# Performance work log

Hardware: AMD Instinct MI355X
Metric: run time of the kernel (lower is better)

Reference implementation:

```python
import jax, jax.numpy as jnp
import numpy as np
import math

NUM_HEADS = 20
HEAD_SIZE = 20  # newssize = 400
NEG_INF = -1e9


def setup_inputs() -> dict:
    key = jax.random.key(0)
    ks = jax.random.split(key, 10)
    B, S, L, V, D, M = 512, 100, 30, 50000, 400, 128
    user_click = jax.random.randint(ks[0], (B, S, L), 0, V)
    seq_len = jax.random.randint(ks[1], (B,), 1, S + 1)  # at least 1 valid click
    sc = 1.0 / math.sqrt(D)
    return {
        "user_click": user_click,
        "seq_len": seq_len,
        "emb_table": jax.random.normal(ks[2], (V, D), jnp.float32) * 0.02,
        "wq": jax.random.normal(ks[3], (D, D), jnp.float32) * sc,
        "wk": jax.random.normal(ks[4], (D, D), jnp.float32) * sc,
        "wv": jax.random.normal(ks[5], (D, D), jnp.float32) * sc,
        "fc1_w": jax.random.normal(ks[6], (D, M), jnp.float32) * sc,
        "fc1_b": jnp.zeros((M,), jnp.float32),
        "fc2_w": jax.random.normal(ks[7], (M, 1), jnp.float32) * (1.0 / math.sqrt(M)),
        "fc2_b": jnp.zeros((1,), jnp.float32),
    }


def reference(user_click, seq_len, emb_table, wq, wk, wv, fc1_w, fc1_b, fc2_w, fc2_b):
    B, S, L = user_click.shape
    D = emb_table.shape[1]
    H, Dh = NUM_HEADS, HEAD_SIZE

    # news encoder: mean-pooled token embeddings -> [B, S, D]
    click = jnp.take(emb_table, user_click.reshape(-1, L), axis=0).mean(axis=1)
    click = click.reshape(B, S, D)

    # mask: valid positions get +1.0 (as in the torch code), invalid -1e9
    valid = jnp.arange(S)[None, :] < seq_len[:, None]  # [B, S]
    mask = jnp.where(valid, 1.0, NEG_INF).astype(click.dtype)

    # multi-head self-attention over history
    q = (click @ wq).reshape(B, S, H, Dh).transpose(0, 2, 1, 3)
    k = (click @ wk).reshape(B, S, H, Dh).transpose(0, 2, 1, 3)
    v = (click @ wv).reshape(B, S, H, Dh).transpose(0, 2, 1, 3)
    logits = jnp.einsum("bhqd,bhkd->bhqk", q, k) / math.sqrt(Dh)
    logits = logits + mask[:, None, None, :]
    attn = jax.nn.softmax(logits, axis=-1)
    ctx = jnp.einsum("bhqk,bhkd->bhqd", attn, v)
    ctx = ctx.transpose(0, 2, 1, 3).reshape(B, S, D)  # [B, S, D]

    # additive attention pooling over history positions
    e = jnp.tanh(ctx @ fc1_w + fc1_b)            # [B, S, M]
    alpha = e @ fc2_w + fc2_b + mask[:, :, None]  # [B, S, 1]
    w = jax.nn.softmax(alpha, axis=1)
    return jnp.sum(w * ctx, axis=1)               # [B, D]
```

## Files before the change

### kernel.cpp

```cpp
#include <hip/hip_runtime.h>
#include <hip/hip_bf16.h>

using u16 = unsigned short;
using u32 = unsigned int;

#define BB 512
#define SS 100
#define LL 30
#define DD 400
#define MM 128
#define HH 20
#define DHH 20
#define SLAB 1024000ull

typedef short v8s __attribute__((ext_vector_type(8)));
typedef float v4f __attribute__((ext_vector_type(4)));

__device__ __forceinline__ float lo2f(u32 u) { return __uint_as_float(u << 16); }
__device__ __forceinline__ float hi2f(u32 u) { return __uint_as_float(u & 0xffff0000u); }
__device__ __forceinline__ float bf2f(u16 h) { return __uint_as_float(((u32)h) << 16); }
__device__ __forceinline__ u16 f2bf(float f) {
  u32 u = __float_as_uint(f);
  u += 0x7fffu + ((u >> 16) & 1u);
  return (u16)(u >> 16);
}
__device__ __forceinline__ u32 packf2(float a, float b) {
  return (u32)f2bf(a) | (((u32)f2bf(b)) << 16);
}

__global__ __launch_bounds__(256) void k_cvt(const float* __restrict__ src,
                                             u16* __restrict__ dst, int n4) {
  const int i = blockIdx.x * 256 + threadIdx.x;
  if (i < n4) {
    const float4 v = ((const float4*)src)[i];
    ((uint2*)dst)[i] = make_uint2(packf2(v.x, v.y), packf2(v.z, v.w));
  }
}

__global__ __launch_bounds__(256) void k_warm(const uint4* __restrict__ emb16,
                                              int n16, float* __restrict__ alpha,
                                              int nA, float* __restrict__ sink) {
  const int gid = blockIdx.x * 256 + threadIdx.x;
  const int stride = gridDim.x * 256;
  for (int i = gid; i < nA; i += stride) alpha[i] = 0.f;
  u32 s = 0;
  for (int i = gid; i < n16; i += stride) {
    const uint4 v = emb16[i];
    s += v.x ^ v.y ^ v.z ^ v.w;
  }
  if (s == 0x12345678u) sink[0] = 1.f;
}

__global__ __launch_bounds__(256) void k_trans_all(const float* __restrict__ wq,
    const float* __restrict__ wk, const float* __restrict__ wv,
    const float* __restrict__ f1w, u16* __restrict__ wt, u16* __restrict__ wtf) {
  __shared__ float ts[32][33];
  const int z = blockIdx.z;
  const float* src = (z == 0) ? wq : (z == 1) ? wk : (z == 2) ? wv : f1w;
  u16* dst = (z < 3) ? (wt + (size_t)z * 160000) : wtf;
  const int N = (z < 3) ? 400 : 128;
  const int K = 400;
  const int t = threadIdx.x;
  const int n0 = blockIdx.x * 32, k0 = blockIdx.y * 32;
  const int c = t & 31, r8 = t >> 5;
#pragma unroll
  for (int i = 0; i < 4; ++i) {
    const int k = k0 + r8 + i * 8, n = n0 + c;
    ts[r8 + i * 8][c] = (k < K && n < N) ? src[(size_t)k * N + n] : 0.f;
  }
  __syncthreads();
#pragma unroll
  for (int i = 0; i < 4; ++i) {
    const int n = n0 + r8 + i * 8, k = k0 + c;
    if (n < N && k < K) dst[(size_t)n * K + k] = f2bf(ts[c][r8 + i * 8]);
  }
}

__global__ __launch_bounds__(256) void k_embed(const int* __restrict__ uc,
                                               const u16* __restrict__ emb,
                                               u32* __restrict__ click) {
  const int wave = threadIdx.x >> 6, lane = threadIdx.x & 63;
  const int bs = blockIdx.x * 4 + wave;
  __shared__ int rows[4][LL];
  if (lane < LL) rows[wave][lane] = uc[(size_t)bs * LL + lane];
  __syncthreads();
  float ax[4] = {0.f, 0.f, 0.f, 0.f}, ay[4] = {0.f, 0.f, 0.f, 0.f};
  for (int l = 0; l < LL; ++l) {
    const u32* row = (const u32*)(emb + (size_t)rows[wave][l] * DD);
    const u32 a = row[lane], b = row[lane + 64], c = row[lane + 128];
    ax[0] += lo2f(a); ay[0] += hi2f(a);
    ax[1] += lo2f(b); ay[1] += hi2f(b);
    ax[2] += lo2f(c); ay[2] += hi2f(c);
    if (lane < 8) { const u32 d = row[lane + 192]; ax[3] += lo2f(d); ay[3] += hi2f(d); }
  }
  const float s = 1.0f / (float)LL;
  u32* orow = click + (size_t)bs * 200;
  orow[lane]       = packf2(ax[0] * s, ay[0] * s);
  orow[lane + 64]  = packf2(ax[1] * s, ay[1] * s);
  orow[lane + 128] = packf2(ax[2] * s, ay[2] * s);
  if (lane < 8) orow[lane + 192] = packf2(ax[3] * s, ay[3] * s);
}

__global__ __launch_bounds__(256) void k_qkv_mfma(const u16* __restrict__ A,
    const u16* __restrict__ Wt, u16* __restrict__ qo, u16* __restrict__ ko_,
    u16* __restrict__ vo) {
  __shared__ u16 As[256][40];
  __shared__ u16 Bs[80][40];
  const int t = threadIdx.x;
  const int wave = t >> 6, lane = t & 63;
  const int q = lane >> 4, l16 = lane & 15;
  const int m0 = blockIdx.x * 256;
  const int mat = blockIdx.y / 5, ntile = blockIdx.y % 5;
  const int nb = ntile * 80;
  const u16* Bt = Wt + (size_t)(mat * 400 + nb) * 400;
  u16* O = (mat == 0) ? qo : ((mat == 1) ? ko_ : vo);
  const int mw = wave * 64;

  v4f acc[4][5];
#pragma unroll
  for (int i = 0; i < 4; ++i)
#pragma unroll
    for (int j = 0; j < 5; ++j) acc[i][j] = (v4f){0.f, 0.f, 0.f, 0.f};

  for (int kt = 0; kt < 13; ++kt) {
    const int k0 = kt * 32;
#pragma unroll
    for (int i = 0; i < 4; ++i) {
      const int id = i * 256 + t;
      const int r = id >> 2, ko = (id & 3) * 8;
      uint4 val = make_uint4(0u, 0u, 0u, 0u);
      if (k0 + ko < 400) val = *(const uint4*)&A[(size_t)(m0 + r) * 400 + k0 + ko];
      *(uint4*)&As[r][ko] = val;
    }
#pragma unroll
    for (int i = 0; i < 2; ++i) {
      const int id = i * 256 + t;
      if (id < 320) {
        const int n = id >> 2, ko = (id & 3) * 8;
        uint4 val = make_uint4(0u, 0u, 0u, 0u);
        if (k0 + ko < 400) val = *(const uint4*)&Bt[(size_t)n * 400 + k0 + ko];
        *(uint4*)&Bs[n][ko] = val;
      }
    }
    __syncthreads();
    v8s a[4], b[5];
#pragma unroll
    for (int ms = 0; ms < 4; ++ms) a[ms] = *(const v8s*)&As[mw + ms * 16 + l16][q * 8];
#pragma unroll
    for (int ns = 0; ns < 5; ++ns) b[ns] = *(const v8s*)&Bs[ns * 16 + l16][q * 8];
#pragma unroll
    for (int ms = 0; ms < 4; ++ms)
#pragma unroll
      for (int ns = 0; ns < 5; ++ns)
        acc[ms][ns] = __builtin_amdgcn_mfma_f32_16x16x32_bf16(a[ms], b[ns], acc[ms][ns], 0, 0, 0);
    __syncthreads();
  }
#pragma unroll
  for (int ms = 0; ms < 4; ++ms)
#pragma unroll
    for (int ns = 0; ns < 5; ++ns) {
      const v4f c = acc[ms][ns];
      const int col = nb + ns * 16 + l16;
      const int head = col / 20, dh = col % 20;
      u16* Oh = O + (size_t)head * SLAB + dh;
#pragma unroll
      for (int reg = 0; reg < 4; ++reg) {
        const int m = m0 + mw + ms * 16 + q * 4 + reg;
        Oh[(size_t)m * 20] = f2bf(c[reg]);
      }
    }
}

__global__ __launch_bounds__(256) void k_attn_mfma(const u16* __restrict__ qg,
    const u16* __restrict__ kg, const u16* __restrict__ vg,
    const int* __restrict__ seq, u16* __restrict__ ctxg) {
  __shared__ u16 Qs[112][40];
  __shared__ u16 Ks[112][40];
  __shared__ u16 Vs[112][40];
  __shared__ u16 Vt[32][136];
  __shared__ u16 Ss[112][136];
  const int b = blockIdx.x / HH, h = blockIdx.x % HH;
  const int t = threadIdx.x;
  const int wave = t >> 6, lane = t & 63;
  const int quad = lane >> 4, l16 = lane & 15;
  const int len = seq[b];
  const u16* qb = qg + (size_t)h * SLAB + (size_t)b * SS * DHH;
  const u16* kb = kg + (size_t)h * SLAB + (size_t)b * SS * DHH;
  const u16* vb = vg + (size_t)h * SLAB + (size_t)b * SS * DHH;
  for (int id = t; id < 896; id += 256) {
    const int r = id >> 3, ch = id & 7;
    uint2 vq = make_uint2(0u, 0u), vk = vq, vv = vq;
    if (r < 100 && ch < 5) {
      vq = *(const uint2*)(qb + r * DHH + ch * 4);
      vk = *(const uint2*)(kb + r * DHH + ch * 4);
      vv = *(const uint2*)(vb + r * DHH + ch * 4);
    }
    *(uint2*)&Qs[r][ch * 4] = vq;
    *(uint2*)&Ks[r][ch * 4] = vk;
    *(uint2*)&Vs[r][ch * 4] = vv;
  }
  for (int id = t; id < 816; id += 256) ((u32*)&Vt[20][0])[id] = 0u;
  for (int id = t; id < 360; id += 256) {
    const int r = id / 18, c = id % 18;
    *(u32*)&Vt[r][100 + c * 2] = 0u;
  }
  for (int id = t; id < 896; id += 256) {
    const int r = id >> 3, c = id & 7;
    *(u32*)&Ss[r][112 + c * 2] = 0u;
  }
  __syncthreads();
  for (int id = t; id < 2000; id += 256) {
    const int d = id / 100, key = id % 100;
    Vt[d][key] = Vs[key][d];
  }
  const float sc = 0.2236067977499790f;
  for (int mi = 0; mi < 2; ++mi) {
    const int mt = wave + mi * 4;
    if (mt >= 7) break;
    const v8s a = *(const v8s*)&Qs[mt * 16 + l16][quad * 8];
    v4f acc[7];
#pragma unroll
    for (int nt = 0; nt < 7; ++nt) {
      const v8s bk = *(const v8s*)&Ks[nt * 16 + l16][quad * 8];
      acc[nt] = __builtin_amdgcn_mfma_f32_16x16x32_bf16(a, bk, (v4f){0.f,0.f,0.f,0.f}, 0, 0, 0);
    }
#pragma unroll
    for (int reg = 0; reg < 4; ++reg) {
      float v[7];
      float mx = -3.0e38f;
#pragma unroll
      for (int nt = 0; nt < 7; ++nt) {
        const int col = nt * 16 + l16;
        v[nt] = acc[nt][reg] * sc + ((col < len) ? 1.0f : -1e9f);
        mx = fmaxf(mx, v[nt]);
      }
#pragma unroll
      for (int o = 1; o < 16; o <<= 1) mx = fmaxf(mx, __shfl_xor(mx, o));
      float sum = 0.f;
#pragma unroll
      for (int nt = 0; nt < 7; ++nt) { v[nt] = __expf(v[nt] - mx); sum += v[nt]; }
#pragma unroll
      for (int o = 1; o < 16; o <<= 1) sum += __shfl_xor(sum, o);
      const float inv = 1.0f / sum;
      const int row = mt * 16 + quad * 4 + reg;
#pragma unroll
      for (int nt = 0; nt < 7; ++nt) Ss[row][nt * 16 + l16] = f2bf(v[nt] * inv);
    }
  }
  __syncthreads();
  u16* cb = ctxg + (size_t)b * SS * DD + h * DHH;
  for (int mi = 0; mi < 2; ++mi) {
    const int mt = wave + mi * 4;
    if (mt >= 7) break;
    v4f o0 = (v4f){0.f,0.f,0.f,0.f}, o1 = o0;
#pragma unroll
    for (int kc = 0; kc < 4; ++kc) {
      const v8s a  = *(const v8s*)&Ss[mt * 16 + l16][kc * 32 + quad * 8];
      const v8s b0 = *(const v8s*)&Vt[l16][kc * 32 + quad * 8];
      const v8s b1 = *(const v8s*)&Vt[16 + l16][kc * 32 + quad * 8];
      o0 = __builtin_amdgcn_mfma_f32_16x16x32_bf16(a, b0, o0, 0, 0, 0);
      o1 = __builtin_amdgcn_mfma_f32_16x16x32_bf16(a, b1, o1, 0, 0, 0);
    }
#pragma unroll
    for (int reg = 0; reg < 4; ++reg) {
      const int q = mt * 16 + quad * 4 + reg;
      if (q < 100) {
        cb[(size_t)q * DD + l16] = f2bf(o0[reg]);
        if (l16 < 4) cb[(size_t)q * DD + 16 + l16] = f2bf(o1[reg]);
      }
    }
  }
}

__global__ __launch_bounds__(256) void k_fc1_alpha(const u16* __restrict__ A,
    const u16* __restrict__ Bt, const float* __restrict__ f1b,
    const float* __restrict__ f2w, float* __restrict__ alpha) {
  __shared__ u16 As[128][40];
  __shared__ u16 Bs[64][40];
  const int t = threadIdx.x;
  const int wave = t >> 6, lane = t & 63;
  const int quad = lane >> 4, l16 = lane & 15;
  const int m0 = blockIdx.x * 128;
  const int nb = blockIdx.y * 64;
  const int mw = wave * 32;
  v4f acc[2][4];
#pragma unroll
  for (int i = 0; i < 2; ++i)
#pragma unroll
    for (int j = 0; j < 4; ++j) acc[i][j] = (v4f){0.f, 0.f, 0.f, 0.f};

  for (int kt = 0; kt < 13; ++kt) {
    const int k0 = kt * 32;
#pragma unroll
    for (int i = 0; i < 2; ++i) {
      const int id = i * 256 + t;
      const int r = id >> 2, ko = (id & 3) * 8;
      uint4 val = make_uint4(0u, 0u, 0u, 0u);
      if (k0 + ko < 400) val = *(const uint4*)&A[(size_t)(m0 + r) * 400 + k0 + ko];
      *(uint4*)&As[r][ko] = val;
    }
    {
      const int r = t >> 2, ko = (t & 3) * 8;
      uint4 val = make_uint4(0u, 0u, 0u, 0u);
      if (k0 + ko < 400) val = *(const uint4*)&Bt[(size_t)(nb + r) * 400 + k0 + ko];
      *(uint4*)&Bs[r][ko] = val;
    }
    __syncthreads();
    v8s a[2], b[4];
#pragma unroll
    for (int ms = 0; ms < 2; ++ms) a[ms] = *(const v8s*)&As[mw + ms * 16 + l16][quad * 8];
#pragma unroll
    for (int ns = 0; ns < 4; ++ns) b[ns] = *(const v8s*)&Bs[ns * 16 + l16][quad * 8];
#pragma unroll
    for (int ms = 0; ms < 2; ++ms)
#pragma unroll
      for (int ns = 0; ns < 4; ++ns)
        acc[ms][ns] = __builtin_amdgcn_mfma_f32_16x16x32_bf16(a[ms], b[ns], acc[ms][ns], 0, 0, 0);
    __syncthreads();
  }
  float fwv[4], fbv[4];
#pragma unroll
  for (int ns = 0; ns < 4; ++ns) {
    fwv[ns] = f2w[nb + ns * 16 + l16];
    fbv[ns] = f1b[nb + ns * 16 + l16];
  }
#pragma unroll
  for (int ms = 0; ms < 2; ++ms)
#pragma unroll
    for (int reg = 0; reg < 4; ++reg) {
      float p = 0.f;
#pragma unroll
      for (int ns = 0; ns < 4; ++ns)
        p += tanhf(acc[ms][ns][reg] + fbv[ns]) * fwv[ns];
#pragma unroll
      for (int o = 1; o < 16; o <<= 1) p += __shfl_xor(p, o);
      if (l16 == 0)
        atomicAdd(&alpha[m0 + mw + ms * 16 + quad * 4 + reg], p);
    }
}

__global__ __launch_bounds__(256) void k_pool(const float* __restrict__ alpha,
    const float* __restrict__ f2b, const int* __restrict__ seq,
    const u16* __restrict__ ctxg, float* __restrict__ out) {
  const int b = blockIdx.x;
  const int t = threadIdx.x, w = t >> 6, lane = t & 63;
  __shared__ float wts[SS];
  const int len = seq[b];
  const float bias = f2b[0];
  if (t < SS) wts[t] = alpha[b * SS + t] + bias + ((t < len) ? 1.0f : -1e9f);
  __syncthreads();
  if (w == 0) {
    const float v0 = wts[lane];
    const float v1 = (lane + 64 < SS) ? wts[lane + 64] : -3.0e38f;
    float mx = fmaxf(v0, v1);
#pragma unroll
    for (int o = 32; o > 0; o >>= 1) mx = fmaxf(mx, __shfl_xor(mx, o));
    const float e0 = __expf(v0 - mx);
    const float e1 = (lane + 64 < SS) ? __expf(v1 - mx) : 0.f;
    float sm = e0 + e1;
#pragma unroll
    for (int o = 32; o > 0; o >>= 1) sm += __shfl_xor(sm, o);
    const float inv = 1.0f / sm;
    wts[lane] = e0 * inv;
    if (lane + 64 < SS) wts[lane + 64] = e1 * inv;
  }
  __syncthreads();
  for (int d = t; d < DD; d += 256) {
    float acc = 0.f;
    const u16* cb = ctxg + (size_t)b * SS * DD + d;
    for (int s = 0; s < SS; ++s) acc += wts[s] * bf2f(cb[(size_t)s * DD]);
    out[(size_t)b * DD + d] = acc;
  }
}

extern "C" void kernel_launch(void* const* d_in, const int* in_sizes, int n_in,
                              void* d_out, int out_size, void* d_ws, size_t ws_size,
                              hipStream_t stream) {
  const int*   uc  = (const int*)d_in[0];
  const int*   seq = (const int*)d_in[1];
  const float* emb = (const float*)d_in[2];
  const float* wq  = (const float*)d_in[3];
  const float* wk  = (const float*)d_in[4];
  const float* wv  = (const float*)d_in[5];
  const float* f1w = (const float*)d_in[6];
  const float* f1b = (const float*)d_in[7];
  const float* f2w = (const float*)d_in[8];
  const float* f2b = (const float*)d_in[9];
  float* out = (float*)d_out;

  u16* emb16   = (u16*)d_ws;
  u16* wt      = emb16 + 20000000ull;
  u16* wtf     = wt + 480000ull;
  u16* click16 = wtf + 51200ull;
  u16* q16     = click16 + 20480000ull;
  u16* k16     = q16 + 20480000ull;
  u16* v16     = k16 + 20480000ull;
  float* alpha = (float*)(v16 + 20480000ull);
  float* sink  = alpha + 51200ull;

  k_cvt<<<(5000000 + 255) / 256, 256, 0, stream>>>(emb, emb16, 5000000);
  k_warm<<<2560, 256, 0, stream>>>((const uint4*)emb16, 2500000, alpha, 51200, sink);
  k_trans_all<<<dim3(13, 13, 4), 256, 0, stream>>>(wq, wk, wv, f1w, wt, wtf);
  k_embed<<<12800, 256, 0, stream>>>(uc, emb16, (u32*)click16);
  k_qkv_mfma<<<dim3(200, 15), 256, 0, stream>>>(click16, wt, q16, k16, v16);
  k_attn_mfma<<<BB * HH, 256, 0, stream>>>(q16, k16, v16, seq, click16);
  k_fc1_alpha<<<dim3(400, 2), 256, 0, stream>>>(click16, wtf, f1b, f2w, alpha);
  k_pool<<<BB, 256, 0, stream>>>(alpha, f2b, seq, click16, out);
}
```

Before: 642.2 us.

## Split bf16 embedding table into column slices for cache-local gather

Converts the fp32 embedding table into eight column slices of 25 packed bf16 pairs each, stored slice-major, and rewrites the gather kernel so each block handles one slice for 20 history items. The aim is to keep each slice's working set small enough to stay resident in cache during the random-row gather, and to order blocks so all eight slices of a chunk run together. The cost is that each gathered row now yields only 100 contiguous bytes per slice, which is less efficient per access. The warm-up kernel is also reordered to run after the weight transpose and to walk the slices.

After: 623.2 us. 1.03x faster.

```diff
diff --git a/kernel.cpp b/kernel.cpp
--- a/kernel.cpp
+++ b/kernel.cpp
@@ -28,24 +28,29 @@
   return (u32)f2bf(a) | (((u32)f2bf(b)) << 16);
 }
 
-__global__ __launch_bounds__(256) void k_cvt(const float* __restrict__ src,
-                                             u16* __restrict__ dst, int n4) {
-  const int i = blockIdx.x * 256 + threadIdx.x;
-  if (i < n4) {
-    const float4 v = ((const float4*)src)[i];
-    ((uint2*)dst)[i] = make_uint2(packf2(v.x, v.y), packf2(v.z, v.w));
-  }
-}
-
-__global__ __launch_bounds__(256) void k_warm(const uint4* __restrict__ emb16,
-                                              int n16, float* __restrict__ alpha,
-                                              int nA, float* __restrict__ sink) {
+__global__ __launch_bounds__(256) void k_slice(const float* __restrict__ emb,
+                                               u32* __restrict__ embS) {
+  const int tid = blockIdx.x * 256 + threadIdx.x;
+  if (tid >= 10000000) return;
+  const int c = tid % 25;
+  const int row = (tid / 25) % 50000;
+  const int slice = tid / (25 * 50000);
+  const float2 v = *(const float2*)&emb[(size_t)row * DD + (slice * 25 + c) * 2];
+  embS[tid] = packf2(v.x, v.y);
+}
+
+__global__ __launch_bounds__(256) void k_warm(const uint4* __restrict__ embS4,
+                                              float* __restrict__ alpha,
+                                              float* __restrict__ sink) {
+  const int slice = blockIdx.x & 7;
+  const int blk = blockIdx.x >> 3;
   const int gid = blockIdx.x * 256 + threadIdx.x;
-  const int stride = gridDim.x * 256;
-  for (int i = gid; i < nA; i += stride) alpha[i] = 0.f;
+  const int gstride = gridDim.x * 256;
+  for (int i = gid; i < 51200; i += gstride) alpha[i] = 0.f;
   u32 s = 0;
-  for (int i = gid; i < n16; i += stride) {
-    const uint4 v = emb16[i];
+  const int base = slice * 312500;
+  for (int i = blk * 256 + threadIdx.x; i < 312500; i += 320 * 256) {
+    const uint4 v = embS4[base + i];
     s += v.x ^ v.y ^ v.z ^ v.w;
   }
   if (s == 0x12345678u) sink[0] = 1.f;
@@ -76,29 +81,32 @@
   }
 }
 
-__global__ __launch_bounds__(256) void k_embed(const int* __restrict__ uc,
-                                               const u16* __restrict__ emb,
-                                               u32* __restrict__ click) {
-  const int wave = threadIdx.x >> 6, lane = threadIdx.x & 63;
-  const int bs = blockIdx.x * 4 + wave;
-  __shared__ int rows[4][LL];
-  if (lane < LL) rows[wave][lane] = uc[(size_t)bs * LL + lane];
-  __syncthreads();
-  float ax[4] = {0.f, 0.f, 0.f, 0.f}, ay[4] = {0.f, 0.f, 0.f, 0.f};
+__global__ __launch_bounds__(256) void k_embed_s(const int* __restrict__ uc,
+                                                 const u32* __restrict__ embS,
+                                                 u32* __restrict__ click) {
+  __shared__ int sIdx[600];
+  const int slice = blockIdx.x & 7;
+  const int chunk = blockIdx.x >> 3;
+  const int bs0 = chunk * 20;
+  const int t = threadIdx.x;
+  for (int i = t; i < 600; i += 256) sIdx[i] = uc[(size_t)bs0 * LL + i];
+  __syncthreads();
+  if (t >= 250) return;
+  const int g = t / 25, c = t % 25;
+  const u32* base = embS + (size_t)slice * 50000u * 25u + c;
+  float a0 = 0.f, a1 = 0.f, b0 = 0.f, b1 = 0.f;
+  const int* i0 = &sIdx[g * 30];
+  const int* i1 = &sIdx[(g + 10) * 30];
+#pragma unroll 6
   for (int l = 0; l < LL; ++l) {
-    const u32* row = (const u32*)(emb + (size_t)rows[wave][l] * DD);
-    const u32 a = row[lane], b = row[lane + 64], c = row[lane + 128];
-    ax[0] += lo2f(a); ay[0] += hi2f(a);
-    ax[1] += lo2f(b); ay[1] += hi2f(b);
-    ax[2] += lo2f(c); ay[2] += hi2f(c);
-    if (lane < 8) { const u32 d = row[lane + 192]; ax[3] += lo2f(d); ay[3] += hi2f(d); }
+    const u32 v0 = base[(size_t)i0[l] * 25];
+    const u32 v1 = base[(size_t)i1[l] * 25];
+    a0 += lo2f(v0); a1 += hi2f(v0);
+    b0 += lo2f(v1); b1 += hi2f(v1);
   }
   const float s = 1.0f / (float)LL;
-  u32* orow = click + (size_t)bs * 200;
-  orow[lane]       = packf2(ax[0] * s, ay[0] * s);
-  orow[lane + 64]  = packf2(ax[1] * s, ay[1] * s);
-  orow[lane + 128] = packf2(ax[2] * s, ay[2] * s);
-  if (lane < 8) orow[lane + 192] = packf2(ax[3] * s, ay[3] * s);
+  click[(size_t)(bs0 + g) * 200 + slice * 25 + c]      = packf2(a0 * s, a1 * s);
+  click[(size_t)(bs0 + g + 10) * 200 + slice * 25 + c] = packf2(b0 * s, b1 * s);
 }
 
 __global__ __launch_bounds__(256) void k_qkv_mfma(const u16* __restrict__ A,
@@ -388,8 +396,8 @@
   const float* f2b = (const float*)d_in[9];
   float* out = (float*)d_out;
 
-  u16* emb16   = (u16*)d_ws;
-  u16* wt      = emb16 + 20000000ull;
+  u32* embS    = (u32*)d_ws;
+  u16* wt      = (u16*)d_ws + 20000000ull;
   u16* wtf     = wt + 480000ull;
   u16* click16 = wtf + 51200ull;
   u16* q16     = click16 + 20480000ull;
@@ -398,10 +406,10 @@
   float* alpha = (float*)(v16 + 20480000ull);
   float* sink  = alpha + 51200ull;
 
-  k_cvt<<<(5000000 + 255) / 256, 256, 0, stream>>>(emb, emb16, 5000000);
-  k_warm<<<2560, 256, 0, stream>>>((const uint4*)emb16, 2500000, alpha, 51200, sink);
+  k_slice<<<39063, 256, 0, stream>>>(emb, embS);
   k_trans_all<<<dim3(13, 13, 4), 256, 0, stream>>>(wq, wk, wv, f1w, wt, wtf);
-  k_embed<<<12800, 256, 0, stream>>>(uc, emb16, (u32*)click16);
+  k_warm<<<2560, 256, 0, stream>>>((const uint4*)embS, alpha, sink);
+  k_embed_s<<<20480, 256, 0, stream>>>(uc, embS, (u32*)click16);
   k_qkv_mfma<<<dim3(200, 15), 256, 0, stream>>>(click16, wt, q16, k16, v16);
   k_attn_mfma<<<BB * HH, 256, 0, stream>>>(q16, k16, v16, seq, click16);
   k_fc1_alpha<<<dim3(400, 2), 256, 0, stream>>>(click16, wtf, f1b, f2w, alpha);
```
